# Optimization experiments

Hardware: AMD Instinct MI355X
Metric: run time of the kernel (lower is better)

The kernel has to match this reference:

```python
import jax, jax.numpy as jnp
import numpy as np

HEADS, DH = 8, 64
DIM = HEADS * DH
ONION, SC = 15, 4
N_VELO, N_SURF = 28504, 3682
N = N_VELO + N_SURF
SURF_KEEP = 3586  # = 16 + (N_SURF - 112)
FIRST_LAP = 500
NT = (ONION + 1) * SC  # 64 tokens
SCALE = DH ** -0.5
EPS = 1e-5


def _attend(tok, Wq, Wk, Wv):
    # tok: [B,H,T,D]
    q, k, v = tok @ Wq, tok @ Wk, tok @ Wv
    a = jax.nn.softmax(jnp.einsum('bhqd,bhkd->bhqk', q, k) * SCALE, axis=-1)
    return jnp.einsum('bhqk,bhkd->bhqd', a, v)


def setup_inputs() -> dict:
    rng = np.random.default_rng(0)
    perm = rng.permutation(N)
    surf_idx = jnp.asarray(np.sort(perm[:N_SURF]), jnp.int32)
    velo_idx = jnp.asarray(np.sort(perm[N_SURF:]), jnp.int32)
    # onion layer labels: first 500 velo points are lap 0 (exactly 500 ones in row 0)
    onion_lab = np.concatenate([np.zeros(FIRST_LAP, np.int64),
                                rng.integers(1, ONION, N_VELO - FIRST_LAP)])
    onion_index = jnp.asarray((onion_lab[None] == np.arange(ONION)[:, None]).astype(np.float32))
    first_lap_idx = jnp.arange(FIRST_LAP, dtype=jnp.int32)
    closest_idx = jnp.asarray(rng.integers(0, SURF_KEEP, N_VELO), jnp.int32)
    labels = jnp.asarray(rng.integers(0, SC, SURF_KEEP), jnp.int32)
    ks = iter(jax.random.split(jax.random.key(0), 32))
    p = lambda shape: jax.random.normal(next(ks), shape, jnp.float32) * 0.02
    z = lambda n: jnp.zeros((n,), jnp.float32)
    x = jax.random.normal(next(ks), (1, N, DIM), jnp.float32)
    return dict(
        x=x, onion_index=onion_index,
        W_fx=p((DIM, DIM)), b_fx=z(DIM),
        W_x=p((DIM, DIM)), b_x=z(DIM),
        Wq1=p((DH, DH)), Wk1=p((DH, DH)), Wv1=p((DH, DH)),
        Wq=p((DH, DH)), Wk=p((DH, DH)), Wv=p((DH, DH)),
        gamma=jnp.ones((NT,), jnp.float32), beta=z(NT),
        W_ws=p((DIM, SC)), b_ws=z(SC),
        W_vv=p((DIM, ONION * SC)), b_vv=z(ONION * SC),
        W_vc=p((DIM, ONION * SC)), b_vc=z(ONION * SC),
        W_out=p((DIM, DIM)), b_out=z(DIM),
        surf_idx=surf_idx, velo_idx=velo_idx, first_lap_idx=first_lap_idx,
        closest_idx=closest_idx, labels=labels)


def reference(x, onion_index, W_fx, b_fx, W_x, b_x, Wq1, Wk1, Wv1, Wq, Wk, Wv,
              gamma, beta, W_ws, b_ws, W_vv, b_vv, W_vc, b_vc, W_out, b_out,
              surf_idx, velo_idx, first_lap_idx, closest_idx, labels):
    B = x.shape[0]
    fx = x @ W_fx + b_fx                                   # in_project_fx
    surf_fx = fx[:, surf_idx]                              # [B,N_SURF,DIM]
    velo_fx = fx[:, velo_idx]                              # [B,N_VELO,DIM]
    # ---- coarse attention: first onion lap + all surface points ----
    fl = velo_fx[:, first_lap_idx]                         # [B,500,DIM]
    tok1 = jnp.concatenate([fl, surf_fx], axis=1)
    tok1 = tok1.reshape(B, -1, HEADS, DH).transpose(0, 2, 1, 3)
    out1 = _attend(tok1, Wq1, Wk1, Wv1)
    velo_first_lap = out1[:, :, :FIRST_LAP].transpose(0, 2, 1, 3).reshape(B, FIRST_LAP, DIM)
    surf_first_lap = out1[:, :, FIRST_LAP:].transpose(0, 2, 1, 3).reshape(B, N_SURF, DIM)
    # ---- fine attention: cluster-mask mean pooling expressed as segment-mean einsum ----
    velo_cluster = labels[closest_idx]                     # [N_VELO]
    onehot_v = (velo_cluster[None] == jnp.arange(SC)[:, None]).astype(fx.dtype)   # [SC,N_VELO]
    # == torch: (velo_fx * onion_mask * cluster_mask).mean(over all N_VELO points)
    new_velo_tokens = jnp.einsum('lp,cp,bpd->blcd', onion_index, onehot_v, velo_fx) / N_VELO
    new_velo_tokens = new_velo_tokens.reshape(B, ONION * SC, DIM)
    surf_keep = jnp.concatenate([surf_fx[:, :16], surf_fx[:, 112:]], axis=1)      # [B,3586,DIM]
    onehot_s = (labels[None] == jnp.arange(SC)[:, None]).astype(fx.dtype)
    surf_tokens = jnp.einsum('cp,bpd->bcd', onehot_s, surf_keep) / SURF_KEEP
    tokens = jnp.concatenate([surf_tokens, new_velo_tokens], axis=1)              # [B,NT,DIM]
    # LayerNorm over the TOKEN axis (torch permutes to [B,DIM,NT] then LayerNorm(NT))
    t = tokens.transpose(0, 2, 1)
    mu = t.mean(-1, keepdims=True)
    var = ((t - mu) ** 2).mean(-1, keepdims=True)
    tokens = ((t - mu) / jnp.sqrt(var + EPS) * gamma + beta).transpose(0, 2, 1)
    tok = tokens.reshape(B, NT, HEADS, DH).transpose(0, 2, 1, 3)
    out_tok = _attend(tok, Wq, Wk, Wv)                     # [B,H,NT,DH]
    # ---- T2P ----
    xm = x @ W_x + b_x                                     # in_project_x
    surf_x = xm[:, surf_idx]
    velo_x = xm[:, velo_idx]
    out_surf = out_tok[:, :, :SC].reshape(B, SC, DIM)      # raw row-major reshape, as in torch
    feat_surf = (surf_x @ W_ws + b_ws) @ out_surf
    out_velo = out_tok[:, :, SC:].transpose(0, 2, 1, 3).reshape(B, ONION * SC, DIM)
    feat_velo = (velo_x @ W_vv + b_vv) @ out_velo
    feat_velo_car = (surf_x @ W_vc + b_vc) @ out_velo
    feat_surf = (feat_surf + feat_velo_car) / 2.0 + surf_first_lap
    feat_velo = feat_velo.at[:, first_lap_idx].add(velo_first_lap)
    new_feature = jnp.zeros_like(x)
    new_feature = new_feature.at[:, surf_idx].set(feat_surf)
    new_feature = new_feature.at[:, velo_idx].set(feat_velo)
    return new_feature @ W_out + b_out                     # to_out
```

## Files before the change

kernel.cpp:

```cpp
#include <hip/hip_runtime.h>

#define N_TOT 32186
#define NV    28504
#define NS    3682
#define DIM   512
#define HEADS 8
#define DH    64
#define FL    500
#define NQ1   4182
#define NQP   4224
#define SK    3586
#define NTOK  64
#define ONION 15
#define SC    4
#define SCALE 0.125f
#define EPS   1e-5f

typedef unsigned short u16;
typedef __bf16 bf16x8 __attribute__((ext_vector_type(8)));
typedef float  f32x4  __attribute__((ext_vector_type(4)));

static __device__ inline void bsplit(float f, u16& hi, u16& lo) {
    __bf16 h = (__bf16)f;
    __bf16 l = (__bf16)(f - (float)h);
    hi = __builtin_bit_cast(u16, h);
    lo = __builtin_bit_cast(u16, l);
}
static __device__ inline uint2 pk2(const u16* s) {
    uint2 w;
    w.x = (unsigned)s[0] | ((unsigned)s[1] << 16);
    w.y = (unsigned)s[2] | ((unsigned)s[3] << 16);
    return w;
}

__global__ __launch_bounds__(256) void k_split_wT(
    const float* __restrict__ W0, const float* __restrict__ W1, const float* __restrict__ W2,
    u16* __restrict__ h0, u16* __restrict__ l0,
    u16* __restrict__ h1, u16* __restrict__ l1,
    u16* __restrict__ h2, u16* __restrict__ l2)
{
    const float* W = (blockIdx.z == 0) ? W0 : (blockIdx.z == 1) ? W1 : W2;
    u16* th = (blockIdx.z == 0) ? h0 : (blockIdx.z == 1) ? h1 : h2;
    u16* tl = (blockIdx.z == 0) ? l0 : (blockIdx.z == 1) ? l1 : l2;
    __shared__ float T[32][33];
    const int tid = threadIdx.x;
    const int k0 = blockIdx.x*32, n0 = blockIdx.y*32;
    {
        int r = tid >> 3, c = (tid & 7) << 2;
        *(float4*)&T[r][c] = *(const float4*)(W + (size_t)(k0+r)*512 + n0 + c);
    }
    __syncthreads();
    int n = tid >> 3, kk = (tid & 7) << 2;
    u16 hh[4], ll[4];
    #pragma unroll
    for (int j = 0; j < 4; ++j) bsplit(T[kk+j][n], hh[j], ll[j]);
    *(uint2*)(th + (size_t)(n0+n)*512 + k0 + kk) = pk2(hh);
    *(uint2*)(tl + (size_t)(n0+n)*512 + k0 + kk) = pk2(ll);
}

__global__ __launch_bounds__(256) void k_mm_bf16s(const float* __restrict__ A,
    const u16* __restrict__ Bth, const u16* __restrict__ Btl,
    const float* __restrict__ bias, float* __restrict__ C, int M)
{
    __shared__ __align__(16) u16 Ash[128][72], Asl[128][72];
    __shared__ __align__(16) u16 Bsh[64][72],  Bsl[64][72];
    const int tid = threadIdx.x;
    const int wave = tid >> 6, lane = tid & 63;
    const int m = lane & 15, quad = lane >> 4;
    const int bn = blockIdx.x * 64;
    const int bm = blockIdx.y * 128;
    const int wm = wave * 32;

    const int ar = tid >> 1;
    const int ac = (tid & 1) << 5;
    const int br = tid >> 2;
    const int bc = (tid & 3) << 4;

    f32x4 acc[2][4];
    #pragma unroll
    for (int mt = 0; mt < 2; ++mt)
        #pragma unroll
        for (int nt = 0; nt < 4; ++nt)
            #pragma unroll
            for (int r = 0; r < 4; ++r) acc[mt][nt][r] = 0.f;

    float4 pa[8];
    uint4 pbh[2], pbl[2];
    {
        bool va = (bm + ar) < M;
        const float* ap = A + (size_t)(bm+ar)*512 + ac;
        #pragma unroll
        for (int u = 0; u < 8; ++u)
            pa[u] = va ? *(const float4*)(ap + u*4) : float4{0,0,0,0};
        size_t bb = (size_t)(bn+br)*512 + bc;
        pbh[0] = *(const uint4*)(Bth + bb); pbh[1] = *(const uint4*)(Bth + bb + 8);
        pbl[0] = *(const uint4*)(Btl + bb); pbl[1] = *(const uint4*)(Btl + bb + 8);
    }

    for (int k0 = 0; k0 < 512; k0 += 64) {
        __syncthreads();
        #pragma unroll
        for (int u = 0; u < 8; ++u) {
            u16 hh[4], ll[4];
            bsplit(pa[u].x, hh[0], ll[0]);
            bsplit(pa[u].y, hh[1], ll[1]);
            bsplit(pa[u].z, hh[2], ll[2]);
            bsplit(pa[u].w, hh[3], ll[3]);
            *(uint2*)&Ash[ar][ac + u*4] = pk2(hh);
            *(uint2*)&Asl[ar][ac + u*4] = pk2(ll);
        }
        *(uint4*)&Bsh[br][bc]   = pbh[0];  *(uint4*)&Bsh[br][bc+8] = pbh[1];
        *(uint4*)&Bsl[br][bc]   = pbl[0];  *(uint4*)&Bsl[br][bc+8] = pbl[1];
        __syncthreads();
        const int kn = k0 + 64;
        if (kn < 512) {
            bool va = (bm + ar) < M;
            const float* ap = A + (size_t)(bm+ar)*512 + kn + ac;
            #pragma unroll
            for (int u = 0; u < 8; ++u)
                pa[u] = va ? *(const float4*)(ap + u*4) : float4{0,0,0,0};
            size_t bb = (size_t)(bn+br)*512 + kn + bc;
            pbh[0] = *(const uint4*)(Bth + bb); pbh[1] = *(const uint4*)(Bth + bb + 8);
            pbl[0] = *(const uint4*)(Btl + bb); pbl[1] = *(const uint4*)(Btl + bb + 8);
        }
        #pragma unroll
        for (int ks = 0; ks < 2; ++ks) {
            bf16x8 ah[2], al[2];
            #pragma unroll
            for (int mt = 0; mt < 2; ++mt) {
                ah[mt] = *(const bf16x8*)&Ash[wm + mt*16 + m][ks*32 + quad*8];
                al[mt] = *(const bf16x8*)&Asl[wm + mt*16 + m][ks*32 + quad*8];
            }
            bf16x8 bh[4], bl[4];
            #pragma unroll
            for (int nt = 0; nt < 4; ++nt) {
                bh[nt] = *(const bf16x8*)&Bsh[nt*16 + m][ks*32 + quad*8];
                bl[nt] = *(const bf16x8*)&Bsl[nt*16 + m][ks*32 + quad*8];
            }
            #pragma unroll
            for (int mt = 0; mt < 2; ++mt)
                #pragma unroll
                for (int nt = 0; nt < 4; ++nt)
                    acc[mt][nt] = __builtin_amdgcn_mfma_f32_16x16x32_bf16(ah[mt], bh[nt], acc[mt][nt], 0,0,0);
            #pragma unroll
            for (int mt = 0; mt < 2; ++mt)
                #pragma unroll
                for (int nt = 0; nt < 4; ++nt)
                    acc[mt][nt] = __builtin_amdgcn_mfma_f32_16x16x32_bf16(ah[mt], bl[nt], acc[mt][nt], 0,0,0);
            #pragma unroll
            for (int mt = 0; mt < 2; ++mt)
                #pragma unroll
                for (int nt = 0; nt < 4; ++nt)
                    acc[mt][nt] = __builtin_amdgcn_mfma_f32_16x16x32_bf16(al[mt], bh[nt], acc[mt][nt], 0,0,0);
        }
    }

    #pragma unroll
    for (int mt = 0; mt < 2; ++mt)
        #pragma unroll
        for (int nt = 0; nt < 4; ++nt) {
            float bsv = bias[bn + nt*16 + m];
            #pragma unroll
            for (int r = 0; r < 4; ++r) {
                int row = bm + wm + mt*16 + quad*4 + r;
                if (row < M)
                    C[(size_t)row*512 + bn + nt*16 + m] = acc[mt][nt][r] + bsv;
            }
        }
}

__global__ __launch_bounds__(256) void k_qkv1(const float* __restrict__ fx,
    const int* __restrict__ surf_idx, const int* __restrict__ velo_idx,
    const int* __restrict__ first_lap,
    const float* __restrict__ Wq, const float* __restrict__ Wk, const float* __restrict__ Wv,
    u16* __restrict__ Qhi, u16* __restrict__ Qlo,
    u16* __restrict__ Khi, u16* __restrict__ Klo,
    u16* __restrict__ Vthi, u16* __restrict__ Vtlo)
{
    __shared__ __align__(16) float As[16][64];
    __shared__ __align__(16) float Bs[3][16][64];
    const int tid = threadIdx.x;
    const int h = blockIdx.y;
    const int r0 = blockIdx.x * 64;
    const int tx = tid & 15, ty = tid >> 4;
    const int lr = tid >> 2, lc = (tid & 3) << 2;
    const int rr = r0 + lr;
    long src = -1;
    if (rr < NQ1) src = (rr < FL) ? velo_idx[first_lap[rr]] : surf_idx[rr - FL];
    float acc[3][4][4] = {};
    for (int k0 = 0; k0 < 64; k0 += 16) {
        float4 av = {0,0,0,0};
        if (src >= 0) av = *(const float4*)(fx + (size_t)src*512 + h*64 + k0 + lc);
        As[lc+0][lr]=av.x; As[lc+1][lr]=av.y; As[lc+2][lr]=av.z; As[lc+3][lr]=av.w;
        const int wr = tid >> 4, wc = (tid & 15) << 2;
        *(float4*)&Bs[0][wr][wc] = *(const float4*)(Wq + (k0+wr)*64 + wc);
        *(float4*)&Bs[1][wr][wc] = *(const float4*)(Wk + (k0+wr)*64 + wc);
        *(float4*)&Bs[2][wr][wc] = *(const float4*)(Wv + (k0+wr)*64 + wc);
        __syncthreads();
        #pragma unroll
        for (int kk = 0; kk < 16; ++kk) {
            float4 a = *(const float4*)&As[kk][ty<<2];
            const float aa[4] = {a.x,a.y,a.z,a.w};
            #pragma unroll
            for (int mm = 0; mm < 3; ++mm) {
                float4 bv = *(const float4*)&Bs[mm][kk][tx<<2];
                const float bb[4] = {bv.x,bv.y,bv.z,bv.w};
                #pragma unroll
                for (int i = 0; i < 4; ++i)
                    #pragma unroll
                    for (int j = 0; j < 4; ++j)
                        acc[mm][i][j] = fmaf(aa[i], bb[j], acc[mm][i][j]);
            }
        }
        __syncthreads();
    }
    #pragma unroll
    for (int i = 0; i < 4; ++i) {
        int r = r0 + (ty<<2) + i;
        size_t qb = ((size_t)h*NQP + r)*64 + (tx<<2);
        u16 qh_[4], ql_[4], kh_[4], kl_[4];
        #pragma unroll
        for (int j = 0; j < 4; ++j) {
            bsplit(acc[0][i][j]*SCALE, qh_[j], ql_[j]);
            bsplit(acc[1][i][j],       kh_[j], kl_[j]);
        }
        *(uint2*)(Qhi + qb) = pk2(qh_);
        *(uint2*)(Qlo + qb) = pk2(ql_);
        *(uint2*)(Khi + qb) = pk2(kh_);
        *(uint2*)(Klo + qb) = pk2(kl_);
        #pragma unroll
        for (int j = 0; j < 4; ++j) {
            u16 vh_, vl_;
            bsplit(acc[2][i][j], vh_, vl_);
            size_t vb = ((size_t)h*64 + (tx<<2) + j)*NQP + r;
            Vthi[vb] = vh_;
            Vtlo[vb] = vl_;
        }
    }
}

__global__ __launch_bounds__(320) void k_attn1(
    const u16* __restrict__ Qhi, const u16* __restrict__ Qlo,
    const u16* __restrict__ Khi, const u16* __restrict__ Klo,
    const u16* __restrict__ Vthi, const u16* __restrict__ Vtlo,
    float* __restrict__ O)
{
    __shared__ __align__(16) u16 Ksh[64][72];
    __shared__ __align__(16) u16 Ksl[64][72];
    __shared__ __align__(16) u16 Vsh[64][72];
    __shared__ __align__(16) u16 Vsl[64][72];
    __shared__ __align__(16) float Ps[5][32*68];

    const int tid = threadIdx.x;
    const int wave = tid >> 6;
    const int lane = tid & 63;
    const int m = lane & 15, quad = lane >> 4;
    const int h = blockIdx.y;
    const int q0 = blockIdx.x*160 + wave*32;

    const u16* Kgh = Khi + (size_t)h*NQP*64;
    const u16* Kgl = Klo + (size_t)h*NQP*64;
    const u16* Vgh = Vthi + (size_t)h*64*NQP;
    const u16* Vgl = Vtlo + (size_t)h*64*NQP;

    bf16x8 qh[2][2], ql[2][2];
    #pragma unroll
    for (int t = 0; t < 2; ++t)
        #pragma unroll
        for (int ks = 0; ks < 2; ++ks) {
            int q = q0 + t*16 + m;
            if (q < NQP) {
                size_t off = ((size_t)h*NQP + q)*64 + ks*32 + quad*8;
                qh[t][ks] = *(const bf16x8*)(Qhi + off);
                ql[t][ks] = *(const bf16x8*)(Qlo + off);
            } else {
                #pragma unroll
                for (int j = 0; j < 8; ++j) { qh[t][ks][j] = (__bf16)0.f; ql[t][ks][j] = (__bf16)0.f; }
            }
        }

    const int sr = tid >> 2;
    const int sc = (tid & 3) << 4;
    uint4 pre[8];
    if (tid < 256) {
        size_t kb = (size_t)sr*64 + sc;
        pre[0] = *(const uint4*)(Kgh + kb);     pre[1] = *(const uint4*)(Kgh + kb + 8);
        pre[2] = *(const uint4*)(Kgl + kb);     pre[3] = *(const uint4*)(Kgl + kb + 8);
        size_t vb = (size_t)sr*NQP + sc;
        pre[4] = *(const uint4*)(Vgh + vb);     pre[5] = *(const uint4*)(Vgh + vb + 8);
        pre[6] = *(const uint4*)(Vgl + vb);     pre[7] = *(const uint4*)(Vgl + vb + 8);
    }

    f32x4 Oc[2][4];
    float mrun[2][4], lrun[2][4];
    #pragma unroll
    for (int t = 0; t < 2; ++t)
        #pragma unroll
        for (int r = 0; r < 4; ++r) {
            mrun[t][r] = -1e30f; lrun[t][r] = 0.f;
            #pragma unroll
            for (int dt = 0; dt < 4; ++dt) Oc[t][dt][r] = 0.f;
        }
    float* Pw = &Ps[wave][0];

    for (int k0 = 0; k0 < NQ1; k0 += 64) {
        __syncthreads();
        if (tid < 256) {
            *(uint4*)&Ksh[sr][sc] = pre[0];  *(uint4*)&Ksh[sr][sc+8] = pre[1];
            *(uint4*)&Ksl[sr][sc] = pre[2];  *(uint4*)&Ksl[sr][sc+8] = pre[3];
            *(uint4*)&Vsh[sr][sc] = pre[4];  *(uint4*)&Vsh[sr][sc+8] = pre[5];
            *(uint4*)&Vsl[sr][sc] = pre[6];  *(uint4*)&Vsl[sr][sc+8] = pre[7];
        }
        __syncthreads();
        const int kn = k0 + 64;
        if (kn < NQ1 && tid < 256) {
            size_t kb = ((size_t)kn + sr)*64 + sc;
            pre[0] = *(const uint4*)(Kgh + kb);     pre[1] = *(const uint4*)(Kgh + kb + 8);
            pre[2] = *(const uint4*)(Kgl + kb);     pre[3] = *(const uint4*)(Kgl + kb + 8);
            size_t vb = (size_t)sr*NQP + kn + sc;
            pre[4] = *(const uint4*)(Vgh + vb);     pre[5] = *(const uint4*)(Vgh + vb + 8);
            pre[6] = *(const uint4*)(Vgl + vb);     pre[7] = *(const uint4*)(Vgl + vb + 8);
        }

        f32x4 S[2][4];
        #pragma unroll
        for (int t = 0; t < 2; ++t)
            #pragma unroll
            for (int n = 0; n < 4; ++n)
                #pragma unroll
                for (int r = 0; r < 4; ++r) S[t][n][r] = 0.f;
        #pragma unroll
        for (int ks = 0; ks < 2; ++ks) {
            bf16x8 kh[4], kl[4];
            #pragma unroll
            for (int n = 0; n < 4; ++n) {
                kh[n] = *(const bf16x8*)&Ksh[n*16 + m][ks*32 + quad*8];
                kl[n] = *(const bf16x8*)&Ksl[n*16 + m][ks*32 + quad*8];
            }
            #pragma unroll
            for (int t = 0; t < 2; ++t)
                #pragma unroll
                for (int n = 0; n < 4; ++n)
                    S[t][n] = __builtin_amdgcn_mfma_f32_16x16x32_bf16(qh[t][ks], kh[n], S[t][n], 0,0,0);
            #pragma unroll
            for (int t = 0; t < 2; ++t)
                #pragma unroll
                for (int n = 0; n < 4; ++n)
                    S[t][n] = __builtin_amdgcn_mfma_f32_16x16x32_bf16(qh[t][ks], kl[n], S[t][n], 0,0,0);
            #pragma unroll
            for (int t = 0; t < 2; ++t)
                #pragma unroll
                for (int n = 0; n < 4; ++n)
                    S[t][n] = __builtin_amdgcn_mfma_f32_16x16x32_bf16(ql[t][ks], kh[n], S[t][n], 0,0,0);
        }
        if (kn > NQ1) {
            #pragma unroll
            for (int n = 0; n < 4; ++n)
                if (k0 + n*16 + m >= NQ1) {
                    #pragma unroll
                    for (int t = 0; t < 2; ++t)
                        #pragma unroll
                        for (int r = 0; r < 4; ++r) S[t][n][r] = -1e30f;
                }
        }

        float alpha[2][4];
        #pragma unroll
        for (int t = 0; t < 2; ++t) {
            float sm[4];
            #pragma unroll
            for (int r = 0; r < 4; ++r) {
                float v = fmaxf(fmaxf(S[t][0][r], S[t][1][r]), fmaxf(S[t][2][r], S[t][3][r]));
                v = fmaxf(v, __shfl_xor(v, 1));
                v = fmaxf(v, __shfl_xor(v, 2));
                v = fmaxf(v, __shfl_xor(v, 4));
                v = fmaxf(v, __shfl_xor(v, 8));
                float mn = fmaxf(mrun[t][r], v);
                alpha[t][r] = __expf(mrun[t][r] - mn);
                mrun[t][r] = mn;
                sm[r] = 0.f;
            }
            #pragma unroll
            for (int n = 0; n < 4; ++n)
                #pragma unroll
                for (int r = 0; r < 4; ++r) {
                    float p = __expf(S[t][n][r] - mrun[t][r]);
                    S[t][n][r] = p;
                    sm[r] += p;
                }
            #pragma unroll
            for (int r = 0; r < 4; ++r) {
                float v = sm[r];
                v += __shfl_xor(v, 1);
                v += __shfl_xor(v, 2);
                v += __shfl_xor(v, 4);
                v += __shfl_xor(v, 8);
                lrun[t][r] = lrun[t][r]*alpha[t][r] + v;
            }
        }
        #pragma unroll
        for (int t = 0; t < 2; ++t)
            #pragma unroll
            for (int dt = 0; dt < 4; ++dt)
                #pragma unroll
                for (int r = 0; r < 4; ++r) Oc[t][dt][r] *= alpha[t][r];

        #pragma unroll
        for (int t = 0; t < 2; ++t)
            #pragma unroll
            for (int n = 0; n < 4; ++n)
                #pragma unroll
                for (int r = 0; r < 4; ++r)
                    Pw[(t*16 + quad*4 + r)*68 + n*16 + m] = S[t][n][r];

        #pragma unroll
        for (int ks = 0; ks < 2; ++ks) {
            bf16x8 ah[2], al[2];
            #pragma unroll
            for (int t = 0; t < 2; ++t) {
                const float* pp = Pw + (t*16 + m)*68 + ks*32 + quad*8;
                float4 xa = *(const float4*)pp;
                float4 xb = *(const float4*)(pp + 4);
                float e0[8] = {xa.x, xa.y, xa.z, xa.w, xb.x, xb.y, xb.z, xb.w};
                #pragma unroll
                for (int j = 0; j < 8; ++j) {
                    __bf16 hb = (__bf16)e0[j];
                    ah[t][j] = hb;
                    al[t][j] = (__bf16)(e0[j] - (float)hb);
                }
            }
            bf16x8 vh[4], vl[4];
            #pragma unroll
            for (int dt = 0; dt < 4; ++dt) {
                vh[dt] = *(const bf16x8*)&Vsh[dt*16 + m][ks*32 + quad*8];
                vl[dt] = *(const bf16x8*)&Vsl[dt*16 + m][ks*32 + quad*8];
            }
            #pragma unroll
            for (int t = 0; t < 2; ++t)
                #pragma unroll
                for (int dt = 0; dt < 4; ++dt)
                    Oc[t][dt] = __builtin_amdgcn_mfma_f32_16x16x32_bf16(ah[t], vh[dt], Oc[t][dt], 0,0,0);
            #pragma unroll
            for (int t = 0; t < 2; ++t)
                #pragma unroll
                for (int dt = 0; dt < 4; ++dt)
                    Oc[t][dt] = __builtin_amdgcn_mfma_f32_16x16x32_bf16(ah[t], vl[dt], Oc[t][dt], 0,0,0);
            #pragma unroll
            for (int t = 0; t < 2; ++t)
                #pragma unroll
                for (int dt = 0; dt < 4; ++dt)
                    Oc[t][dt] = __builtin_amdgcn_mfma_f32_16x16x32_bf16(al[t], vh[dt], Oc[t][dt], 0,0,0);
        }
    }

    #pragma unroll
    for (int t = 0; t < 2; ++t) {
        float il[4];
        #pragma unroll
        for (int r = 0; r < 4; ++r) il[r] = 1.f / lrun[t][r];
        #pragma unroll
        for (int dt = 0; dt < 4; ++dt)
            #pragma unroll
            for (int r = 0; r < 4; ++r) {
                int q = q0 + t*16 + quad*4 + r;
                if (q < NQ1)
                    O[((size_t)h*NQ1 + q)*64 + dt*16 + m] = Oc[t][dt][r] * il[r];
            }
    }
}

__global__ void k_bucket_prep(const int* __restrict__ labels, const int* __restrict__ closest,
    const int* __restrict__ surf_idx, const int* __restrict__ velo_idx,
    const float* __restrict__ onion, int* __restrict__ tok_of, int* __restrict__ src_of)
{
    int r = blockIdx.x*256 + threadIdx.x;
    if (r < SK) {
        tok_of[r] = labels[r];
        int s = (r < 16) ? r : r + 96;
        src_of[r] = surf_idx[s];
    } else if (r < SK + NV) {
        int p = r - SK;
        int cl = labels[closest[p]];
        int l = 0;
        #pragma unroll
        for (int q = 1; q < ONION; ++q)
            if (onion[(size_t)q*NV + p] != 0.f) l = q;
        tok_of[r] = SC + l*SC + cl;
        src_of[r] = velo_idx[p];
    }
}

__global__ __launch_bounds__(256) void k_tokens_accum(const float* __restrict__ fx,
    const int* __restrict__ tok_of, const int* __restrict__ src_of, float* __restrict__ part)
{
    __shared__ float acc[64][256];
    const int tid = threadIdx.x;
    for (int i = tid; i < 64*256; i += 256) ((float*)acc)[i] = 0.f;
    __syncthreads();
    const int d0 = blockIdx.x << 8;
    const int R = SK + NV;
    const int per = (R + gridDim.y - 1) / gridDim.y;
    int rs = blockIdx.y * per;
    int re = rs + per; if (re > R) re = R;
    const float wS = 1.f / SK, wV = 1.f / NV;
    int r = rs;
    for (; r + 4 <= re; r += 4) {
        int t0 = tok_of[r], t1 = tok_of[r+1], t2 = tok_of[r+2], t3 = tok_of[r+3];
        int s0 = src_of[r], s1 = src_of[r+1], s2 = src_of[r+2], s3 = src_of[r+3];
        float v0 = fx[(size_t)s0*512 + d0 + tid] * ((r   < SK) ? wS : wV);
        float v1 = fx[(size_t)s1*512 + d0 + tid] * ((r+1 < SK) ? wS : wV);
        float v2 = fx[(size_t)s2*512 + d0 + tid] * ((r+2 < SK) ? wS : wV);
        float v3 = fx[(size_t)s3*512 + d0 + tid] * ((r+3 < SK) ? wS : wV);
        acc[t0][tid] += v0; acc[t1][tid] += v1; acc[t2][tid] += v2; acc[t3][tid] += v3;
    }
    for (; r < re; ++r) {
        float v = fx[(size_t)src_of[r]*512 + d0 + tid] * ((r < SK) ? wS : wV);
        acc[tok_of[r]][tid] += v;
    }
    __syncthreads();
    float* dst = part + ((size_t)blockIdx.x*gridDim.y + blockIdx.y)*64*256;
    for (int i = tid; i < 64*256; i += 256) dst[i] = acc[i >> 8][i & 255];
}

__global__ void k_tokens_reduce(const float* __restrict__ part, float* __restrict__ tokens)
{
    int idx = blockIdx.x*256 + threadIdx.x;
    int t = idx >> 9;
    int dg = idx & 511;
    int cc = dg >> 8, d = dg & 255;
    float s = 0.f;
    for (int ch = 0; ch < 64; ++ch)
        s += part[(((size_t)cc*64 + ch)*64 + t)*256 + d];
    tokens[idx] = s;
}

__global__ void k_ln(const float* __restrict__ tokens, const float* __restrict__ gamma,
    const float* __restrict__ beta, float* __restrict__ tln)
{
    int ch = blockIdx.x*256 + threadIdx.x;
    if (ch >= 512) return;
    float vals[64];
    float mu = 0.f;
    #pragma unroll
    for (int t = 0; t < 64; ++t) { vals[t] = tokens[t*512 + ch]; mu += vals[t]; }
    mu *= (1.f/64.f);
    float var = 0.f;
    #pragma unroll
    for (int t = 0; t < 64; ++t) { float d = vals[t]-mu; var = fmaf(d, d, var); }
    var *= (1.f/64.f);
    float rstd = rsqrtf(var + EPS);
    #pragma unroll
    for (int t = 0; t < 64; ++t)
        tln[t*512 + ch] = (vals[t]-mu)*rstd*gamma[t] + beta[t];
}

__global__ __launch_bounds__(256) void k_qkv2(const float* __restrict__ tln,
    const float* __restrict__ Wq, const float* __restrict__ Wk, const float* __restrict__ Wv,
    float* __restrict__ q2, float* __restrict__ k2, float* __restrict__ v2)
{
    __shared__ float Ts[64][64];
    __shared__ float Wt[3][64][65];
    const int h = blockIdx.x, tid = threadIdx.x;
    for (int i = tid; i < 4096; i += 256) {
        int t = i >> 6, d = i & 63;
        Ts[t][d] = tln[t*512 + h*64 + d];
    }
    for (int i = tid; i < 4096; i += 256) {
        int d = i >> 6, e = i & 63;
        Wt[0][e][d] = Wq[i]; Wt[1][e][d] = Wk[i]; Wt[2][e][d] = Wv[i];
    }
    __syncthreads();
    for (int o = tid; o < 4096; o += 256) {
        int t = o >> 6, e = o & 63;
        float s0 = 0.f, s1 = 0.f, s2 = 0.f;
        for (int d = 0; d < 64; ++d) {
            float xv = Ts[t][d];
            s0 = fmaf(xv, Wt[0][e][d], s0);
            s1 = fmaf(xv, Wt[1][e][d], s1);
            s2 = fmaf(xv, Wt[2][e][d], s2);
        }
        size_t idx = (size_t)h*4096 + o;
        q2[idx] = s0; k2[idx] = s1; v2[idx] = s2;
    }
}

__global__ __launch_bounds__(256) void k_attn2(const float* __restrict__ q2,
    const float* __restrict__ k2, const float* __restrict__ v2, float* __restrict__ ot)
{
    __shared__ float Qs[64][65], Ks[64][65], Vs[64][65], Ps2[64][65];
    const int h = blockIdx.x, tid = threadIdx.x;
    const float* qh = q2 + (size_t)h*4096;
    const float* kh = k2 + (size_t)h*4096;
    const float* vh = v2 + (size_t)h*4096;
    for (int i = tid; i < 4096; i += 256) {
        int t = i >> 6, e = i & 63;
        Qs[t][e] = qh[i]; Ks[t][e] = kh[i]; Vs[t][e] = vh[i];
    }
    __syncthreads();
    for (int o = tid; o < 4096; o += 256) {
        int t = o >> 6, j = o & 63;
        float s = 0.f;
        for (int e = 0; e < 64; ++e) s = fmaf(Qs[t][e], Ks[j][e], s);
        Ps2[t][j] = s * SCALE;
    }
    __syncthreads();
    if (tid < 64) {
        float mx = -1e30f;
        for (int j = 0; j < 64; ++j) mx = fmaxf(mx, Ps2[tid][j]);
        float sum = 0.f;
        for (int j = 0; j < 64; ++j) { float p = __expf(Ps2[tid][j]-mx); Ps2[tid][j] = p; sum += p; }
        float inv = 1.f / sum;
        for (int j = 0; j < 64; ++j) Ps2[tid][j] *= inv;
    }
    __syncthreads();
    for (int o = tid; o < 4096; o += 256) {
        int t = o >> 6, e = o & 63;
        float s = 0.f;
        for (int j = 0; j < 64; ++j) s = fmaf(Ps2[t][j], Vs[j][e], s);
        ot[(size_t)h*4096 + o] = s;
    }
}

__global__ void k_build_ov(const float* __restrict__ ot, float* __restrict__ osurf,
    float* __restrict__ ovelo)
{
    int i = blockIdx.x*256 + threadIdx.x;
    if (i < 2048) {
        osurf[i] = ot[((i >> 8) << 12) + (i & 255)];
    }
    int g = i - 2048;
    if (g >= 0 && g < 60*512) {
        int j = g >> 9, cch = g & 511;
        int hh = cch >> 6, d = cch & 63;
        ovelo[g] = ot[(size_t)hh*4096 + (SC + j)*64 + d];
    }
}

__global__ __launch_bounds__(256) void k_coef_surf(const float* __restrict__ xm,
    const int* __restrict__ surf_idx,
    const float* __restrict__ W_ws, const float* __restrict__ b_ws,
    const float* __restrict__ W_vc, const float* __restrict__ b_vc,
    float* __restrict__ cs, float* __restrict__ cc)
{
    __shared__ __align__(16) float As[16][516];
    __shared__ float Ws[128][64];
    const int tid = threadIdx.x;
    const int s0 = blockIdx.x * 16;
    for (int i = tid; i < 16*128; i += 256) {
        int r = i >> 7, c4 = (i & 127) << 2;
        float4 a = {0,0,0,0};
        int s = s0 + r;
        if (s < NS) a = *(const float4*)(xm + (size_t)surf_idx[s]*512 + c4);
        *(float4*)&As[r][c4] = a;
    }
    const int c = tid & 63, rg = tid >> 6;
    float acc[4] = {0,0,0,0};
    for (int k0 = 0; k0 < 512; k0 += 128) {
        __syncthreads();
        for (int i = tid; i < 128*64; i += 256) {
            int kk = i >> 6, cw = i & 63;
            int k = k0 + kk;
            Ws[kk][cw] = (cw < 4) ? W_ws[k*4 + cw] : W_vc[k*60 + (cw-4)];
        }
        __syncthreads();
        #pragma unroll 8
        for (int kk = 0; kk < 128; kk += 4) {
            float w0 = Ws[kk][c], w1 = Ws[kk+1][c], w2 = Ws[kk+2][c], w3 = Ws[kk+3][c];
            #pragma unroll
            for (int u = 0; u < 4; ++u) {
                float4 a = *(const float4*)&As[rg + (u<<2)][k0 + kk];
                acc[u] = fmaf(a.x,w0, fmaf(a.y,w1, fmaf(a.z,w2, fmaf(a.w,w3, acc[u]))));
            }
        }
    }
    #pragma unroll
    for (int u = 0; u < 4; ++u) {
        int s = s0 + rg + (u<<2);
        if (s >= NS) continue;
        if (c < 4) cs[(size_t)s*4 + c] = acc[u] + b_ws[c];
        else cc[(size_t)s*60 + (c-4)] = acc[u] + b_vc[c-4];
    }
}

__global__ __launch_bounds__(256) void k_coef_velo(const float* __restrict__ xm,
    const int* __restrict__ velo_idx, const float* __restrict__ W,
    const float* __restrict__ b, float* __restrict__ cv)
{
    __shared__ __align__(16) float As[16][516];
    __shared__ float Ws[128][64];
    const int tid = threadIdx.x;
    const int v0 = blockIdx.x * 16;
    for (int i = tid; i < 16*128; i += 256) {
        int r = i >> 7, c4 = (i & 127) << 2;
        float4 a = {0,0,0,0};
        int v = v0 + r;
        if (v < NV) a = *(const float4*)(xm + (size_t)velo_idx[v]*512 + c4);
        *(float4*)&As[r][c4] = a;
    }
    const int c = tid & 63, rg = tid >> 6;
    float acc[4] = {0,0,0,0};
    for (int k0 = 0; k0 < 512; k0 += 128) {
        __syncthreads();
        for (int i = tid; i < 128*64; i += 256) {
            int kk = i >> 6, cw = i & 63;
            Ws[kk][cw] = (cw < 60) ? W[(size_t)(k0+kk)*60 + cw] : 0.f;
        }
        __syncthreads();
        #pragma unroll 8
        for (int kk = 0; kk < 128; kk += 4) {
            float w0 = Ws[kk][c], w1 = Ws[kk+1][c], w2 = Ws[kk+2][c], w3 = Ws[kk+3][c];
            #pragma unroll
            for (int u = 0; u < 4; ++u) {
                float4 a = *(const float4*)&As[rg + (u<<2)][k0 + kk];
                acc[u] = fmaf(a.x,w0, fmaf(a.y,w1, fmaf(a.z,w2, fmaf(a.w,w3, acc[u]))));
            }
        }
    }
    if (c < 60) {
        float bb = b[c];
        #pragma unroll
        for (int u = 0; u < 4; ++u) {
            int v = v0 + rg + (u<<2);
            if (v < NV) cv[(size_t)v*60 + c] = acc[u] + bb;
        }
    }
}

__global__ __launch_bounds__(256) void k_feat_velo(const float* __restrict__ cv,
    const float* __restrict__ ovelo, const float* __restrict__ O1,
    const int* __restrict__ velo_idx, float* __restrict__ nf)
{
    __shared__ float Cs[16][64];
    const int tid = threadIdx.x;
    const int v0 = blockIdx.x * 16;
    for (int i = tid; i < 16*64; i += 256) {
        int r = i >> 6, j = i & 63;
        int v = v0 + r;
        Cs[r][j] = (j < 60 && v < NV) ? cv[(size_t)v*60 + j] : 0.f;
    }
    __syncthreads();
    const int c = tid, c2 = tid + 256;
    float a0[16], a1[16];
    #pragma unroll
    for (int r = 0; r < 16; ++r) { a0[r] = 0.f; a1[r] = 0.f; }
    #pragma unroll 4
    for (int j = 0; j < 60; ++j) {
        float e0 = ovelo[j*512 + c];
        float e1 = ovelo[j*512 + c2];
        #pragma unroll
        for (int r = 0; r < 16; ++r) {
            float cf = Cs[r][j];
            a0[r] = fmaf(cf, e0, a0[r]);
            a1[r] = fmaf(cf, e1, a1[r]);
        }
    }
    const int h0 = c >> 6, d0 = c & 63, h1 = c2 >> 6, d1 = c2 & 63;
    for (int r = 0; r < 16; ++r) {
        int v = v0 + r;
        if (v >= NV) break;
        float f0 = a0[r], f1 = a1[r];
        if (v < FL) {
            f0 += O1[((size_t)h0*NQ1 + v)*64 + d0];
            f1 += O1[((size_t)h1*NQ1 + v)*64 + d1];
        }
        size_t row = (size_t)velo_idx[v]*512;
        nf[row + c] = f0;
        nf[row + c2] = f1;
    }
}

__global__ __launch_bounds__(256) void k_feat_surf(const float* __restrict__ cs,
    const float* __restrict__ cc, const float* __restrict__ osurf,
    const float* __restrict__ ovelo, const float* __restrict__ O1,
    const int* __restrict__ surf_idx, float* __restrict__ nf)
{
    __shared__ float Cs[16][64];
    const int tid = threadIdx.x;
    const int s0 = blockIdx.x * 16;
    for (int i = tid; i < 16*64; i += 256) {
        int r = i >> 6, j = i & 63;
        int s = s0 + r;
        float v = 0.f;
        if (s < NS) v = (j < 4) ? cs[(size_t)s*4 + j] : cc[(size_t)s*60 + (j-4)];
        Cs[r][j] = v;
    }
    __syncthreads();
    const int c = tid, c2 = tid + 256;
    float a0[16], a1[16];
    #pragma unroll
    for (int r = 0; r < 16; ++r) { a0[r] = 0.f; a1[r] = 0.f; }
    #pragma unroll 4
    for (int j = 0; j < 64; ++j) {
        float e0 = (j < 4) ? osurf[j*512 + c]  : ovelo[(j-4)*512 + c];
        float e1 = (j < 4) ? osurf[j*512 + c2] : ovelo[(j-4)*512 + c2];
        #pragma unroll
        for (int r = 0; r < 16; ++r) {
            float cf = Cs[r][j];
            a0[r] = fmaf(cf, e0, a0[r]);
            a1[r] = fmaf(cf, e1, a1[r]);
        }
    }
    const int h0 = c >> 6, d0 = c & 63, h1 = c2 >> 6, d1 = c2 & 63;
    for (int r = 0; r < 16; ++r) {
        int s = s0 + r;
        if (s >= NS) break;
        float f0 = 0.5f*a0[r] + O1[((size_t)h0*NQ1 + FL + s)*64 + d0];
        float f1 = 0.5f*a1[r] + O1[((size_t)h1*NQ1 + FL + s)*64 + d1];
        size_t row = (size_t)surf_idx[s]*512;
        nf[row + c] = f0;
        nf[row + c2] = f1;
    }
}

extern "C" void kernel_launch(void* const* d_in, const int* in_sizes, int n_in,
                              void* d_out, int out_size, void* d_ws, size_t ws_size,
                              hipStream_t stream)
{
    const float* x       = (const float*)d_in[0];
    const float* onion   = (const float*)d_in[1];
    const float* W_fx    = (const float*)d_in[2];
    const float* b_fx    = (const float*)d_in[3];
    const float* W_x     = (const float*)d_in[4];
    const float* b_x     = (const float*)d_in[5];
    const float* Wq1     = (const float*)d_in[6];
    const float* Wk1     = (const float*)d_in[7];
    const float* Wv1     = (const float*)d_in[8];
    const float* Wq      = (const float*)d_in[9];
    const float* Wk      = (const float*)d_in[10];
    const float* Wv      = (const float*)d_in[11];
    const float* gamma   = (const float*)d_in[12];
    const float* beta    = (const float*)d_in[13];
    const float* W_ws    = (const float*)d_in[14];
    const float* b_ws    = (const float*)d_in[15];
    const float* W_vv    = (const float*)d_in[16];
    const float* b_vv    = (const float*)d_in[17];
    const float* W_vc    = (const float*)d_in[18];
    const float* b_vc    = (const float*)d_in[19];
    const float* W_out   = (const float*)d_in[20];
    const float* b_out   = (const float*)d_in[21];
    const int* surf_idx  = (const int*)d_in[22];
    const int* velo_idx  = (const int*)d_in[23];
    const int* first_lap = (const int*)d_in[24];
    const int* closest   = (const int*)d_in[25];
    const int* labels    = (const int*)d_in[26];
    float* out = (float*)d_out;
    float* ws  = (float*)d_ws;

    size_t o = 0;
    float* fx   = ws + o;  o += (size_t)N_TOT*512;
    float* xm   = ws + o;  o += (size_t)N_TOT*512;
    float* O1   = ws + o;  o += (size_t)HEADS*NQ1*64;
    const size_t BFSZ = (size_t)HEADS*NQP*64/2;
    u16* Qhi = (u16*)(ws + o); o += BFSZ;
    u16* Qlo = (u16*)(ws + o); o += BFSZ;
    u16* Khi = (u16*)(ws + o); o += BFSZ;
    u16* Klo = (u16*)(ws + o); o += BFSZ;
    u16* Vthi= (u16*)(ws + o); o += BFSZ;
    u16* Vtlo= (u16*)(ws + o); o += BFSZ;
    const size_t WSPL = (size_t)512*512/2;
    u16* Wfxh = (u16*)(ws + o); o += WSPL;
    u16* Wfxl = (u16*)(ws + o); o += WSPL;
    u16* Wxh  = (u16*)(ws + o); o += WSPL;
    u16* Wxl  = (u16*)(ws + o); o += WSPL;
    u16* Woh  = (u16*)(ws + o); o += WSPL;
    u16* Wol  = (u16*)(ws + o); o += WSPL;
    float* tokens = ws + o; o += 64*512;
    float* tln  = ws + o;  o += 64*512;
    float* q2   = ws + o;  o += 8*64*64;
    float* k2   = ws + o;  o += 8*64*64;
    float* v2   = ws + o;  o += 8*64*64;
    float* ot   = ws + o;  o += 8*64*64;
    float* osurf= ws + o;  o += 4*512;
    float* ovelo= ws + o;  o += 60*512;
    float* cs   = ws + o;  o += (size_t)NS*4;
    float* cv   = ws + o;  o += (size_t)NV*60;
    float* cc   = ws + o;  o += (size_t)NS*60;
    int* tok_of = (int*)(ws + o); o += SK + NV;
    int* src_of = (int*)(ws + o); o += SK + NV;
    float* part = ws + o;  o += (size_t)2*64*64*256;
    float* nf = fx;

    (void)in_sizes; (void)n_in; (void)out_size; (void)ws_size;

    k_split_wT<<<dim3(16,16,3), 256, 0, stream>>>(W_fx, W_x, W_out,
                                                  Wfxh, Wfxl, Wxh, Wxl, Woh, Wol);
    k_mm_bf16s<<<dim3(8, 252), 256, 0, stream>>>(x, Wfxh, Wfxl, b_fx, fx, N_TOT);
    k_mm_bf16s<<<dim3(8, 252), 256, 0, stream>>>(x, Wxh,  Wxl,  b_x,  xm, N_TOT);
    k_bucket_prep<<<126, 256, 0, stream>>>(labels, closest, surf_idx, velo_idx, onion, tok_of, src_of);
    k_qkv1<<<dim3(66, 8), 256, 0, stream>>>(fx, surf_idx, velo_idx, first_lap, Wq1, Wk1, Wv1,
                                            Qhi, Qlo, Khi, Klo, Vthi, Vtlo);
    k_attn1<<<dim3(27, 8), 320, 0, stream>>>(Qhi, Qlo, Khi, Klo, Vthi, Vtlo, O1);
    k_tokens_accum<<<dim3(2, 64), 256, 0, stream>>>(fx, tok_of, src_of, part);
    k_tokens_reduce<<<128, 256, 0, stream>>>(part, tokens);
    k_ln<<<2, 256, 0, stream>>>(tokens, gamma, beta, tln);
    k_qkv2<<<8, 256, 0, stream>>>(tln, Wq, Wk, Wv, q2, k2, v2);
    k_attn2<<<8, 256, 0, stream>>>(q2, k2, v2, ot);
    k_build_ov<<<128, 256, 0, stream>>>(ot, osurf, ovelo);
    k_coef_surf<<<231, 256, 0, stream>>>(xm, surf_idx, W_ws, b_ws, W_vc, b_vc, cs, cc);
    k_coef_velo<<<1782, 256, 0, stream>>>(xm, velo_idx, W_vv, b_vv, cv);
    k_feat_velo<<<1782, 256, 0, stream>>>(cv, ovelo, O1, velo_idx, nf);
    k_feat_surf<<<231, 256, 0, stream>>>(cs, cc, osurf, ovelo, O1, surf_idx, nf);
    k_mm_bf16s<<<dim3(8, 252), 256, 0, stream>>>(nf, Woh, Wol, b_out, out, N_TOT);
}
```

Baseline: 1.304 ms.

## Split first attention over key range with flash-decoding style merge

The first attention kernel now splits the key dimension into two halves across a third grid dimension and shrinks blocks from 5 to 4 waves. Each half writes unnormalised partial outputs plus running max and sum, and a new merge kernel combines them. The grid grows from 216 to 528 blocks to fill more compute units on the GPU. The cost is extra global traffic for the partial outputs and an additional kernel launch.

Result: no change. 1.317 ms (+1.0%).

```diff
diff --git a/kernel.cpp b/kernel.cpp
--- a/kernel.cpp
+++ b/kernel.cpp
@@ -9,6 +9,7 @@
 #define FL    500
 #define NQ1   4182
 #define NQP   4224
+#define KSPL  2112
 #define SK    3586
 #define NTOK  64
 #define ONION 15
@@ -239,24 +240,30 @@
     }
 }
 
-__global__ __launch_bounds__(320) void k_attn1(
+__global__ __launch_bounds__(256) void k_attn1(
     const u16* __restrict__ Qhi, const u16* __restrict__ Qlo,
     const u16* __restrict__ Khi, const u16* __restrict__ Klo,
     const u16* __restrict__ Vthi, const u16* __restrict__ Vtlo,
-    float* __restrict__ O)
+    float* __restrict__ Op0, float* __restrict__ Op1,
+    float2* __restrict__ Ml0, float2* __restrict__ Ml1)
 {
     __shared__ __align__(16) u16 Ksh[64][72];
     __shared__ __align__(16) u16 Ksl[64][72];
     __shared__ __align__(16) u16 Vsh[64][72];
     __shared__ __align__(16) u16 Vsl[64][72];
-    __shared__ __align__(16) float Ps[5][32*68];
+    __shared__ __align__(16) float Ps[4][32*68];
 
     const int tid = threadIdx.x;
     const int wave = tid >> 6;
     const int lane = tid & 63;
     const int m = lane & 15, quad = lane >> 4;
     const int h = blockIdx.y;
-    const int q0 = blockIdx.x*160 + wave*32;
+    const int q0 = blockIdx.x*128 + wave*32;
+    const int zz = blockIdx.z;
+    const int kbeg = zz ? KSPL : 0;
+    const int kend = zz ? NQ1 : KSPL;
+    float*  Op = zz ? Op1 : Op0;
+    float2* Ml = zz ? Ml1 : Ml0;
 
     const u16* Kgh = Khi + (size_t)h*NQP*64;
     const u16* Kgl = Klo + (size_t)h*NQP*64;
@@ -269,24 +276,19 @@
         #pragma unroll
         for (int ks = 0; ks < 2; ++ks) {
             int q = q0 + t*16 + m;
-            if (q < NQP) {
-                size_t off = ((size_t)h*NQP + q)*64 + ks*32 + quad*8;
-                qh[t][ks] = *(const bf16x8*)(Qhi + off);
-                ql[t][ks] = *(const bf16x8*)(Qlo + off);
-            } else {
-                #pragma unroll
-                for (int j = 0; j < 8; ++j) { qh[t][ks][j] = (__bf16)0.f; ql[t][ks][j] = (__bf16)0.f; }
-            }
+            size_t off = ((size_t)h*NQP + q)*64 + ks*32 + quad*8;
+            qh[t][ks] = *(const bf16x8*)(Qhi + off);
+            ql[t][ks] = *(const bf16x8*)(Qlo + off);
         }
 
     const int sr = tid >> 2;
     const int sc = (tid & 3) << 4;
     uint4 pre[8];
-    if (tid < 256) {
-        size_t kb = (size_t)sr*64 + sc;
+    {
+        size_t kb = ((size_t)kbeg + sr)*64 + sc;
         pre[0] = *(const uint4*)(Kgh + kb);     pre[1] = *(const uint4*)(Kgh + kb + 8);
         pre[2] = *(const uint4*)(Kgl + kb);     pre[3] = *(const uint4*)(Kgl + kb + 8);
-        size_t vb = (size_t)sr*NQP + sc;
+        size_t vb = (size_t)sr*NQP + kbeg + sc;
         pre[4] = *(const uint4*)(Vgh + vb);     pre[5] = *(const uint4*)(Vgh + vb + 8);
         pre[6] = *(const uint4*)(Vgl + vb);     pre[7] = *(const uint4*)(Vgl + vb + 8);
     }
@@ -303,17 +305,15 @@
         }
     float* Pw = &Ps[wave][0];
 
-    for (int k0 = 0; k0 < NQ1; k0 += 64) {
+    for (int k0 = kbeg; k0 < kend; k0 += 64) {
         __syncthreads();
-        if (tid < 256) {
-            *(uint4*)&Ksh[sr][sc] = pre[0];  *(uint4*)&Ksh[sr][sc+8] = pre[1];
-            *(uint4*)&Ksl[sr][sc] = pre[2];  *(uint4*)&Ksl[sr][sc+8] = pre[3];
-            *(uint4*)&Vsh[sr][sc] = pre[4];  *(uint4*)&Vsh[sr][sc+8] = pre[5];
-            *(uint4*)&Vsl[sr][sc] = pre[6];  *(uint4*)&Vsl[sr][sc+8] = pre[7];
-        }
+        *(uint4*)&Ksh[sr][sc] = pre[0];  *(uint4*)&Ksh[sr][sc+8] = pre[1];
+        *(uint4*)&Ksl[sr][sc] = pre[2];  *(uint4*)&Ksl[sr][sc+8] = pre[3];
+        *(uint4*)&Vsh[sr][sc] = pre[4];  *(uint4*)&Vsh[sr][sc+8] = pre[5];
+        *(uint4*)&Vsl[sr][sc] = pre[6];  *(uint4*)&Vsl[sr][sc+8] = pre[7];
         __syncthreads();
         const int kn = k0 + 64;
-        if (kn < NQ1 && tid < 256) {
+        if (kn < kend) {
             size_t kb = ((size_t)kn + sr)*64 + sc;
             pre[0] = *(const uint4*)(Kgh + kb);     pre[1] = *(const uint4*)(Kgh + kb + 8);
             pre[2] = *(const uint4*)(Kgl + kb);     pre[3] = *(const uint4*)(Kgl + kb + 8);
@@ -455,18 +455,43 @@
 
     #pragma unroll
     for (int t = 0; t < 2; ++t) {
-        float il[4];
-        #pragma unroll
-        for (int r = 0; r < 4; ++r) il[r] = 1.f / lrun[t][r];
+        #pragma unroll
+        for (int r = 0; r < 4; ++r) {
+            int q = q0 + t*16 + quad*4 + r;
+            if (q < NQ1 && m == 0)
+                Ml[(size_t)h*NQ1 + q] = make_float2(mrun[t][r], lrun[t][r]);
+        }
         #pragma unroll
         for (int dt = 0; dt < 4; ++dt)
             #pragma unroll
             for (int r = 0; r < 4; ++r) {
                 int q = q0 + t*16 + quad*4 + r;
                 if (q < NQ1)
-                    O[((size_t)h*NQ1 + q)*64 + dt*16 + m] = Oc[t][dt][r] * il[r];
-            }
-    }
+                    Op[((size_t)h*NQ1 + q)*64 + dt*16 + m] = Oc[t][dt][r];
+            }
+    }
+}
+
+__global__ __launch_bounds__(256) void k_attn_merge(
+    const float* __restrict__ Op0, const float* __restrict__ Op1,
+    const float2* __restrict__ Ml0, const float2* __restrict__ Ml1,
+    float* __restrict__ O)
+{
+    int idx = blockIdx.x*256 + threadIdx.x;
+    if (idx >= HEADS*NQ1*16) return;
+    int row = idx >> 4, d4 = (idx & 15) << 2;
+    float2 a = Ml0[row], b = Ml1[row];
+    float mx = fmaxf(a.x, b.x);
+    float e0 = __expf(a.x - mx), e1 = __expf(b.x - mx);
+    float inv = 1.f / (a.y*e0 + b.y*e1);
+    float4 o0 = *(const float4*)(Op0 + (size_t)row*64 + d4);
+    float4 o1 = *(const float4*)(Op1 + (size_t)row*64 + d4);
+    float4 r;
+    r.x = (o0.x*e0 + o1.x*e1)*inv;
+    r.y = (o0.y*e0 + o1.y*e1)*inv;
+    r.z = (o0.z*e0 + o1.z*e1)*inv;
+    r.w = (o0.w*e0 + o1.w*e1)*inv;
+    *(float4*)(O + (size_t)row*64 + d4) = r;
 }
 
 __global__ void k_bucket_prep(const int* __restrict__ labels, const int* __restrict__ closest,
@@ -850,6 +875,9 @@
     float* fx   = ws + o;  o += (size_t)N_TOT*512;
     float* xm   = ws + o;  o += (size_t)N_TOT*512;
     float* O1   = ws + o;  o += (size_t)HEADS*NQ1*64;
+    float* Op1  = ws + o;  o += (size_t)HEADS*NQ1*64;
+    float2* Ml0 = (float2*)(ws + o); o += (size_t)HEADS*NQ1*2;
+    float2* Ml1 = (float2*)(ws + o); o += (size_t)HEADS*NQ1*2;
     const size_t BFSZ = (size_t)HEADS*NQP*64/2;
     u16* Qhi = (u16*)(ws + o); o += BFSZ;
     u16* Qlo = (u16*)(ws + o); o += BFSZ;
@@ -889,7 +917,9 @@
     k_bucket_prep<<<126, 256, 0, stream>>>(labels, closest, surf_idx, velo_idx, onion, tok_of, src_of);
     k_qkv1<<<dim3(66, 8), 256, 0, stream>>>(fx, surf_idx, velo_idx, first_lap, Wq1, Wk1, Wv1,
                                             Qhi, Qlo, Khi, Klo, Vthi, Vtlo);
-    k_attn1<<<dim3(27, 8), 320, 0, stream>>>(Qhi, Qlo, Khi, Klo, Vthi, Vtlo, O1);
+    k_attn1<<<dim3(33, 8, 2), 256, 0, stream>>>(Qhi, Qlo, Khi, Klo, Vthi, Vtlo,
+                                                O1, Op1, Ml0, Ml1);
+    k_attn_merge<<<(HEADS*NQ1*16 + 255)/256, 256, 0, stream>>>(O1, Op1, Ml0, Ml1, O1);
     k_tokens_accum<<<dim3(2, 64), 256, 0, stream>>>(fx, tok_of, src_of, part);
     k_tokens_reduce<<<128, 256, 0, stream>>>(part, tokens);
     k_ln<<<2, 256, 0, stream>>>(tokens, gamma, beta, tln);
```
